# Kernel optimization log

Hardware: AMD Instinct MI355X
Metric: run time of the kernel (lower is better)

Reference implementation:

```python
import jax, jax.numpy as jnp
import numpy as np

N = 16384      # nodes
E = 262144     # edges (avg degree 16)
T = 4          # type_num
D = 64         # d_model
L = 2          # layers


def setup_inputs() -> dict:
    key = jax.random.key(0)
    ks = jax.random.split(key, 7)
    return {
        "x": jax.random.normal(ks[0], (N, D), dtype=jnp.float32),
        "edge_feature": jax.random.normal(ks[1], (T, D), dtype=jnp.float32),
        "theta": jax.random.normal(ks[2], (L, T, 3 * D), dtype=jnp.float32) * (1.0 / np.sqrt(3 * D)),
        "wr": jax.random.normal(ks[3], (L, D, D), dtype=jnp.float32) * (1.0 / np.sqrt(D)),
        "we": jax.random.normal(ks[4], (L, D, D), dtype=jnp.float32) * (1.0 / np.sqrt(D)),
        "edge_index": jax.random.randint(ks[5], (2, E), 0, N, dtype=jnp.int64),
        "edge_type": jax.random.randint(ks[6], (E,), 0, T, dtype=jnp.int64),
    }


def _scatter_softmax(r, row, num_nodes):
    # r: [T, E]; softmax over edges grouped by destination node `row`.
    rT = r.T  # [E, T] (segment ops reduce over leading axis)
    m = jax.ops.segment_max(rT, row, num_segments=num_nodes)   # [N, T]
    e = jnp.exp(rT - m[row])                                    # [E, T]
    s = jax.ops.segment_sum(e, row, num_segments=num_nodes)     # [N, T]
    return (e / s[row]).T                                       # [T, E]


def reference(x, edge_feature, theta, wr, we, edge_index, edge_type):
    n, d = x.shape
    t = edge_feature.shape[0]
    num_layers = theta.shape[0]
    row, col = edge_index[0], edge_index[1]

    h = jnp.broadcast_to(x[None], (t, n, d))  # x.expand(type_num, N, d)
    ef = edge_feature                          # [T, D]
    for i in range(num_layers):
        tg, thi, thj = theta[i, :, :d], theta[i, :, d:2 * d], theta[i, :, 2 * d:]
        # per-edge scores
        r_g = (tg @ ef.T)[:, edge_type]                        # [T, E]
        r_hi = jnp.einsum('tnd,td->tn', h, thi)[:, row]        # [T, E]
        r_hj = jnp.einsum('tnd,td->tn', h, thj)[:, col]        # [T, E]
        r = _scatter_softmax(r_g + r_hi + r_hj, row, n)        # [T, E]
        # gated messages
        ef = ef @ wr[i]                                        # [T, D]
        v_g = jax.nn.sigmoid(ef)[edge_type]                    # [E, D]
        v_h = jnp.einsum('tnd,de->tne', h, we[i])[:, col]      # [T, E, D]
        msg = r[:, :, None] * v_g[None] * v_h                  # [T, E, D]
        agg = jax.ops.segment_sum(jnp.moveaxis(msg, 1, 0), row, num_segments=n)  # [N, T, D]
        h = jnp.moveaxis(agg, 0, 1)                            # [T, N, D]
        if i < num_layers - 1:
            h = jax.nn.relu(h)      # dropout is identity in eval mode
            ef = jax.nn.relu(ef)
    return h
```

## Files before the change

kernel.cpp:

```cpp
#include <hip/hip_runtime.h>

#define NN 16384
#define EE 262144
#define TT 4
#define DD 64
#define SLOT 96
#define HB (EE / 256)
#define NB (NN / 64)

__device__ inline float wave_reduce_max(float v) {
    #pragma unroll
    for (int off = 32; off >= 1; off >>= 1) v = fmaxf(v, __shfl_xor(v, off));
    return v;
}
__device__ inline float wave_reduce_sum(float v) {
    #pragma unroll
    for (int off = 32; off >= 1; off >>= 1) v += __shfl_xor(v, off);
    return v;
}
__device__ inline float4 edge_group_reduce(float4 v) {
    #pragma unroll
    for (int off = 16; off < 64; off <<= 1) {
        v.x += __shfl_xor(v.x, off); v.y += __shfl_xor(v.y, off);
        v.z += __shfl_xor(v.z, off); v.w += __shfl_xor(v.w, off);
    }
    return v;
}
__device__ inline unsigned short f2bf(float f) {
    unsigned u = __float_as_uint(f);
    u += 0x7FFFu + ((u >> 16) & 1u);
    return (unsigned short)(u >> 16);
}
__device__ inline float bf2f(unsigned short h) {
    return __uint_as_float(((unsigned)h) << 16);
}
__device__ inline float4 bf4_to_f4(ushort4 h) {
    return float4{bf2f(h.x), bf2f(h.y), bf2f(h.z), bf2f(h.w)};
}

#define ONL(mm, ss, r) { if ((r) > (mm)) { ss = ss * __expf(mm - (r)) + 1.f; mm = (r); } \
                         else ss += __expf((r) - (mm)); }

__global__ __launch_bounds__(256) void build_node0_kernel(
        const int* __restrict__ row, const int* __restrict__ col,
        const int* __restrict__ et, int* __restrict__ cnt,
        int* __restrict__ ce_slot,
        const float* __restrict__ x, const float* __restrict__ theta,
        const float* __restrict__ we, const float* __restrict__ ef_in,
        const float* __restrict__ wr,
        float* __restrict__ a4, float* __restrict__ b4,
        unsigned short* __restrict__ hw0,
        float* __restrict__ sg, float* __restrict__ rg) {
    __shared__ float h_lds[64][68];
    __shared__ float4 we_lds[64][16];
    __shared__ float th_lds[4][2][64];
    __shared__ float part_a[64][4][4];
    __shared__ float part_b[64][4][4];
    __shared__ float ef0[TT * DD];
    __shared__ float ef1[TT * DD];
    int tid = threadIdx.x;
    int bid = blockIdx.x;

    if (bid < HB) {
        int e = bid * 256 + tid;
        int r = row[e];
        int pos = atomicAdd(&cnt[r], 1);
        if (pos < SLOT)
            ce_slot[r * SLOT + pos] = col[e] | (et[e] << 14);
        return;
    }
    bid -= HB;

    if (bid == NB) {
        int t = tid >> 6, d = tid & 63;
        ef0[tid] = ef_in[tid];
        __syncthreads();
        if (tid < 16) {
            int tt = tid & 3, tq = tid >> 2;
            float s = 0.f;
            for (int k = 0; k < DD; ++k) s += theta[tq * 192 + k] * ef0[tt * DD + k];
            rg[tq * 4 + tt] = s;
        }
        float acc = 0.f;
        for (int k = 0; k < DD; ++k) acc += ef0[t * DD + k] * wr[k * DD + d];
        sg[tid] = 1.f / (1.f + __expf(-acc));
        ef1[tid] = fmaxf(acc, 0.f);
        __syncthreads();
        if (tid < 16) {
            int tt = tid & 3, tq = tid >> 2;
            float s = 0.f;
            for (int k = 0; k < DD; ++k) s += theta[(TT + tq) * 192 + k] * ef1[tt * DD + k];
            rg[16 + tq * 4 + tt] = s;
        }
        float acc2 = 0.f;
        for (int k = 0; k < DD; ++k) acc2 += ef1[t * DD + k] * wr[DD * DD + k * DD + d];
        sg[TT * DD + tid] = 1.f / (1.f + __expf(-acc2));
        return;
    }

    int n0 = bid * 64;
    {
        int q = tid & 15, nr = tid >> 4;
        #pragma unroll
        for (int r = 0; r < 4; ++r) {
            int n = r * 16 + nr;
            *(float4*)&h_lds[n][4 * q] = ((const float4*)x)[(n0 + n) * 16 + q];
        }
    }
    {
        const float4* we4 = (const float4*)we;
        #pragma unroll
        for (int r = 0; r < 4; ++r)
            ((float4*)we_lds)[tid + 256 * r] = we4[tid + 256 * r];
    }
    {
        #pragma unroll
        for (int r = 0; r < 2; ++r) {
            int e = tid + 256 * r;
            int t = e >> 7, ab = (e >> 6) & 1, k = e & 63;
            th_lds[t][ab][k] = theta[t * 192 + 64 + ab * 64 + k];
        }
    }
    __syncthreads();
    int i = tid >> 4, j = tid & 15;
    float4 acc[4];
    acc[0] = acc[1] = acc[2] = acc[3] = float4{0.f, 0.f, 0.f, 0.f};
    for (int k = 0; k < 64; ++k) {
        float4 wv = we_lds[k][j];
        #pragma unroll
        for (int r = 0; r < 4; ++r) {
            float hv = h_lds[4 * i + r][k];
            acc[r].x += hv * wv.x; acc[r].y += hv * wv.y;
            acc[r].z += hv * wv.z; acc[r].w += hv * wv.w;
        }
    }
    {
        int t = j >> 2, kq = j & 3;
        float pa[4] = {0, 0, 0, 0}, pb[4] = {0, 0, 0, 0};
        for (int kk = 0; kk < 16; ++kk) {
            int k = kq * 16 + kk;
            float ti = th_lds[t][0][k], tj = th_lds[t][1][k];
            #pragma unroll
            for (int r = 0; r < 4; ++r) {
                float hv = h_lds[4 * i + r][k];
                pa[r] += hv * ti; pb[r] += hv * tj;
            }
        }
        #pragma unroll
        for (int r = 0; r < 4; ++r) {
            part_a[4 * i + r][t][kq] = pa[r];
            part_b[4 * i + r][t][kq] = pb[r];
        }
    }
    #pragma unroll
    for (int r = 0; r < 4; ++r) {
        ushort4 hv;
        hv.x = f2bf(acc[r].x); hv.y = f2bf(acc[r].y);
        hv.z = f2bf(acc[r].z); hv.w = f2bf(acc[r].w);
        ((ushort4*)hw0)[(n0 + 4 * i + r) * 16 + j] = hv;
    }
    __syncthreads();
    {
        int n = tid >> 2, t = tid & 3;
        float4 va = *(float4*)&part_a[n][t][0];
        float4 vb = *(float4*)&part_b[n][t][0];
        a4[(n0 + n) * 4 + t] = va.x + va.y + va.z + va.w;
        b4[(n0 + n) * 4 + t] = vb.x + vb.y + vb.z + vb.w;
    }
}

__global__ __launch_bounds__(256) void edge_agg0_kernel(
        const int* __restrict__ cnt, const int* __restrict__ ce_slot,
        const float* __restrict__ a4, const float* __restrict__ b4,
        const float* __restrict__ rg, const float* __restrict__ sg,
        const unsigned short* __restrict__ hw0,
        const float* __restrict__ we, const float* __restrict__ theta,
        float* __restrict__ a4o, float* __restrict__ b4o,
        unsigned short* __restrict__ hw1) {
    __shared__ float4 sg4[64];
    __shared__ float4 rg4[4];
    __shared__ int cols[4][SLOT];
    __shared__ float4 wT[4][SLOT];
    __shared__ float h1_lds[16][68];
    __shared__ float th1[4][2][64];
    __shared__ float part_a[16][17];
    __shared__ float part_b[16][17];
    int tid = threadIdx.x;
    if (tid < 64) sg4[tid] = ((const float4*)sg)[tid];
    if (tid < 4)  rg4[tid] = float4{rg[tid], rg[4 + tid], rg[8 + tid], rg[12 + tid]};
    #pragma unroll
    for (int r2 = 0; r2 < 2; ++r2) {
        int e2 = tid + 256 * r2;
        int t2 = e2 >> 7, ab = (e2 >> 6) & 1, k = e2 & 63;
        th1[t2][ab][k] = theta[(TT + t2) * 192 + 64 + ab * 64 + k];
    }
    int w = tid >> 6, lane = tid & 63;
    int n = blockIdx.x * 4 + w;
    int deg = cnt[n]; if (deg > SLOT) deg = SLOT;
    const int* ces = ce_slot + n * SLOT;
    float4 av = ((const float4*)a4)[n];
    __syncthreads();

    float m0 = -INFINITY, m1 = -INFINITY, m2 = -INFINITY, m3 = -INFINITY;
    float s0 = 0.f, s1 = 0.f, s2 = 0.f, s3 = 0.f;
    for (int e = lane; e < deg; e += 64) {
        int pk = ces[e];
        int c = pk & 16383, tt = pk >> 14;
        float4 bv = ((const float4*)b4)[c];
        float4 rv = rg4[tt];
        float4 rp{av.x + bv.x + rv.x, av.y + bv.y + rv.y,
                  av.z + bv.z + rv.z, av.w + bv.w + rv.w};
        cols[w][e] = pk;
        wT[w][e] = rp;
        ONL(m0, s0, rp.x) ONL(m1, s1, rp.y) ONL(m2, s2, rp.z) ONL(m3, s3, rp.w)
    }
    float M0 = wave_reduce_max(m0), M1 = wave_reduce_max(m1);
    float M2 = wave_reduce_max(m2), M3 = wave_reduce_max(m3);
    float S0 = wave_reduce_sum((m0 > -INFINITY) ? s0 * __expf(m0 - M0) : 0.f);
    float S1 = wave_reduce_sum((m1 > -INFINITY) ? s1 * __expf(m1 - M1) : 0.f);
    float S2 = wave_reduce_sum((m2 > -INFINITY) ? s2 * __expf(m2 - M2) : 0.f);
    float S3 = wave_reduce_sum((m3 > -INFINITY) ? s3 * __expf(m3 - M3) : 0.f);
    float i0 = (S0 > 0.f) ? 1.f / S0 : 0.f, i1 = (S1 > 0.f) ? 1.f / S1 : 0.f;
    float i2 = (S2 > 0.f) ? 1.f / S2 : 0.f, i3 = (S3 > 0.f) ? 1.f / S3 : 0.f;
    for (int e = lane; e < deg; e += 64) {
        float4 rp = wT[w][e];
        wT[w][e] = float4{__expf(rp.x - M0) * i0, __expf(rp.y - M1) * i1,
                          __expf(rp.z - M2) * i2, __expf(rp.w - M3) * i3};
    }

    int eg = lane >> 4, q = lane & 15;
    float4 acc0{0,0,0,0}, acc1{0,0,0,0}, acc2{0,0,0,0}, acc3{0,0,0,0};
    const ushort4* hw4 = (const ushort4*)hw0;
    for (int base = 0; base < deg; base += 4) {
        int e = base + eg;
        if (e < deg) {
            int pk = cols[w][e];
            int c = pk & 16383, tt = pk >> 14;
            ushort4 hv = hw4[c * 16 + q];
            float4 sgv = sg4[tt * 16 + q];
            float4 wv = wT[w][e];
            float4 f = bf4_to_f4(hv);
            float4 g{sgv.x * f.x, sgv.y * f.y, sgv.z * f.z, sgv.w * f.w};
            acc0.x += wv.x * g.x; acc0.y += wv.x * g.y; acc0.z += wv.x * g.z; acc0.w += wv.x * g.w;
            acc1.x += wv.y * g.x; acc1.y += wv.y * g.y; acc1.z += wv.y * g.z; acc1.w += wv.y * g.w;
            acc2.x += wv.z * g.x; acc2.y += wv.z * g.y; acc2.z += wv.z * g.z; acc2.w += wv.z * g.w;
            acc3.x += wv.w * g.x; acc3.y += wv.w * g.y; acc3.z += wv.w * g.z; acc3.w += wv.w * g.w;
        }
    }
    acc0 = edge_group_reduce(acc0);
    acc1 = edge_group_reduce(acc1);
    acc2 = edge_group_reduce(acc2);
    acc3 = edge_group_reduce(acc3);
    float4 o = acc0;
    if (eg == 1) o = acc1;
    if (eg == 2) o = acc2;
    if (eg == 3) o = acc3;
    o.x = fmaxf(o.x, 0.f); o.y = fmaxf(o.y, 0.f);
    o.z = fmaxf(o.z, 0.f); o.w = fmaxf(o.w, 0.f);
    *(float4*)&h1_lds[eg * 4 + w][4 * q] = o;
    __syncthreads();

    int r = tid >> 4, j = tid & 15;
    int t1 = r >> 2, wn = r & 3;
    int n1 = blockIdx.x * 4 + wn;
    const float4* we2 = (const float4*)(we + DD * DD);
    float4 ga{0,0,0,0};
    for (int k = 0; k < 64; ++k) {
        float hv = h1_lds[r][k];
        float4 wv = we2[k * 16 + j];
        ga.x += hv * wv.x; ga.y += hv * wv.y;
        ga.z += hv * wv.z; ga.w += hv * wv.w;
    }
    float pa = 0.f, pb = 0.f;
    #pragma unroll
    for (int kk = 0; kk < 4; ++kk) {
        int k = 4 * j + kk;
        float hv = h1_lds[r][k];
        pa += hv * th1[t1][0][k]; pb += hv * th1[t1][1][k];
    }
    part_a[r][j] = pa; part_b[r][j] = pb;
    ushort4 hb;
    hb.x = f2bf(ga.x); hb.y = f2bf(ga.y); hb.z = f2bf(ga.z); hb.w = f2bf(ga.w);
    ((ushort4*)hw1)[((size_t)t1 * NN + n1) * 16 + j] = hb;
    __syncthreads();
    if (tid < 16) {
        float s = 0.f;
        #pragma unroll
        for (int jj = 0; jj < 16; ++jj) s += part_a[tid][jj];
        a4o[(blockIdx.x * 4 + (tid & 3)) * 4 + (tid >> 2)] = s;
    } else if (tid < 32) {
        int r3 = tid - 16;
        float s = 0.f;
        #pragma unroll
        for (int jj = 0; jj < 16; ++jj) s += part_b[r3][jj];
        b4o[(blockIdx.x * 4 + (r3 & 3)) * 4 + (r3 >> 2)] = s;
    }
}

__global__ __launch_bounds__(256) void edge_agg1_kernel(
        const int* __restrict__ cnt, const int* __restrict__ ce_slot,
        const float* __restrict__ a4, const float* __restrict__ b4,
        const float* __restrict__ rg, const float* __restrict__ sg,
        const unsigned short* __restrict__ hw, float* __restrict__ out) {
    __shared__ float4 sg4[64];
    __shared__ float4 rg4[4];
    __shared__ int cols[4][SLOT];
    __shared__ float4 wT[4][SLOT];
    int tid = threadIdx.x;
    if (tid < 64) sg4[tid] = ((const float4*)sg)[tid];
    if (tid < 4)  rg4[tid] = float4{rg[tid], rg[4 + tid], rg[8 + tid], rg[12 + tid]};
    int w = tid >> 6, lane = tid & 63;
    int n = blockIdx.x * 4 + w;
    int deg = cnt[n]; if (deg > SLOT) deg = SLOT;
    const int* ces = ce_slot + n * SLOT;
    float4 av = ((const float4*)a4)[n];
    __syncthreads();

    float m0 = -INFINITY, m1 = -INFINITY, m2 = -INFINITY, m3 = -INFINITY;
    float s0 = 0.f, s1 = 0.f, s2 = 0.f, s3 = 0.f;
    for (int e = lane; e < deg; e += 64) {
        int pk = ces[e];
        int c = pk & 16383, tt = pk >> 14;
        float4 bv = ((const float4*)b4)[c];
        float4 rv = rg4[tt];
        float4 rp{av.x + bv.x + rv.x, av.y + bv.y + rv.y,
                  av.z + bv.z + rv.z, av.w + bv.w + rv.w};
        cols[w][e] = pk;
        wT[w][e] = rp;
        ONL(m0, s0, rp.x) ONL(m1, s1, rp.y) ONL(m2, s2, rp.z) ONL(m3, s3, rp.w)
    }
    float M0 = wave_reduce_max(m0), M1 = wave_reduce_max(m1);
    float M2 = wave_reduce_max(m2), M3 = wave_reduce_max(m3);
    float S0 = wave_reduce_sum((m0 > -INFINITY) ? s0 * __expf(m0 - M0) : 0.f);
    float S1 = wave_reduce_sum((m1 > -INFINITY) ? s1 * __expf(m1 - M1) : 0.f);
    float S2 = wave_reduce_sum((m2 > -INFINITY) ? s2 * __expf(m2 - M2) : 0.f);
    float S3 = wave_reduce_sum((m3 > -INFINITY) ? s3 * __expf(m3 - M3) : 0.f);
    float i0 = (S0 > 0.f) ? 1.f / S0 : 0.f, i1 = (S1 > 0.f) ? 1.f / S1 : 0.f;
    float i2 = (S2 > 0.f) ? 1.f / S2 : 0.f, i3 = (S3 > 0.f) ? 1.f / S3 : 0.f;
    for (int e = lane; e < deg; e += 64) {
        float4 rp = wT[w][e];
        wT[w][e] = float4{__expf(rp.x - M0) * i0, __expf(rp.y - M1) * i1,
                          __expf(rp.z - M2) * i2, __expf(rp.w - M3) * i3};
    }

    int eg = lane >> 4, q = lane & 15;
    float4 acc0{0,0,0,0}, acc1{0,0,0,0}, acc2{0,0,0,0}, acc3{0,0,0,0};
    const ushort4* hw4 = (const ushort4*)hw;
    for (int base = 0; base < deg; base += 4) {
        int e = base + eg;
        if (e < deg) {
            int pk = cols[w][e];
            int c = pk & 16383, tt = pk >> 14;
            int ba = c * 16 + q;
            ushort4 h0 = hw4[ba];
            ushort4 h1v = hw4[NN * 16 + ba];
            ushort4 h2 = hw4[2 * NN * 16 + ba];
            ushort4 h3 = hw4[3 * NN * 16 + ba];
            float4 sgv = sg4[tt * 16 + q];
            float4 wv = wT[w][e];
            float4 f0 = bf4_to_f4(h0), f1 = bf4_to_f4(h1v);
            float4 f2 = bf4_to_f4(h2), f3 = bf4_to_f4(h3);
            acc0.x += wv.x * sgv.x * f0.x; acc0.y += wv.x * sgv.y * f0.y;
            acc0.z += wv.x * sgv.z * f0.z; acc0.w += wv.x * sgv.w * f0.w;
            acc1.x += wv.y * sgv.x * f1.x; acc1.y += wv.y * sgv.y * f1.y;
            acc1.z += wv.y * sgv.z * f1.z; acc1.w += wv.y * sgv.w * f1.w;
            acc2.x += wv.z * sgv.x * f2.x; acc2.y += wv.z * sgv.y * f2.y;
            acc2.z += wv.z * sgv.z * f2.z; acc2.w += wv.z * sgv.w * f2.w;
            acc3.x += wv.w * sgv.x * f3.x; acc3.y += wv.w * sgv.y * f3.y;
            acc3.z += wv.w * sgv.z * f3.z; acc3.w += wv.w * sgv.w * f3.w;
        }
    }
    acc0 = edge_group_reduce(acc0);
    acc1 = edge_group_reduce(acc1);
    acc2 = edge_group_reduce(acc2);
    acc3 = edge_group_reduce(acc3);
    float4 o = acc0;
    if (eg == 1) o = acc1;
    if (eg == 2) o = acc2;
    if (eg == 3) o = acc3;
    ((float4*)out)[(eg * NN + n) * 16 + q] = o;
}

extern "C" void kernel_launch(void* const* d_in, const int* in_sizes, int n_in,
                              void* d_out, int out_size, void* d_ws, size_t ws_size,
                              hipStream_t stream) {
    const float* x     = (const float*)d_in[0];
    const float* ef_in = (const float*)d_in[1];
    const float* theta = (const float*)d_in[2];
    const float* wr    = (const float*)d_in[3];
    const float* we    = (const float*)d_in[4];
    const int* edge_index = (const int*)d_in[5];
    const int* edge_type  = (const int*)d_in[6];
    float* out = (float*)d_out;

    const int* row = edge_index;
    const int* col = edge_index + EE;

    char* p = (char*)d_ws;
    auto alloc = [&](size_t bytes) { void* r = (void*)p; p += (bytes + 255) & ~(size_t)255; return r; };
    int*   cnt     = (int*)  alloc((size_t)NN * 4);
    int*   ce_slot = (int*)  alloc((size_t)NN * SLOT * 4);
    float* a4_0    = (float*)alloc((size_t)NN * 4 * 4);
    float* b4_0    = (float*)alloc((size_t)NN * 4 * 4);
    float* a4_1    = (float*)alloc((size_t)NN * 4 * 4);
    float* b4_1    = (float*)alloc((size_t)NN * 4 * 4);
    unsigned short* hw0 = (unsigned short*)alloc((size_t)NN * DD * 2);
    unsigned short* hw1 = (unsigned short*)alloc((size_t)TT * NN * DD * 2);
    float* sg      = (float*)alloc((size_t)2 * TT * DD * 4);
    float* rg      = (float*)alloc((size_t)2 * 16 * 4);

    hipMemsetAsync(cnt, 0, (size_t)NN * 4, stream);
    build_node0_kernel<<<HB + NB + 1, 256, 0, stream>>>(
        row, col, edge_type, cnt, ce_slot, x, theta, we, ef_in, wr,
        a4_0, b4_0, hw0, sg, rg);
    edge_agg0_kernel<<<NN / 4, 256, 0, stream>>>(
        cnt, ce_slot, a4_0, b4_0, rg, sg, hw0, we, theta, a4_1, b4_1, hw1);
    edge_agg1_kernel<<<NN / 4, 256, 0, stream>>>(
        cnt, ce_slot, a4_1, b4_1, rg + 16, sg + TT * DD, hw1, out);
}
```

Measured before the change: 156.8 us.

## Split layer-1 node transform out of edge aggregation into a tiled kernel

The layer-0 edge aggregation kernel no longer computes the layer-1 node transform (h1·We and the theta projections) inline. It now writes relu'd h1 in fp32 to global memory, and a new node1_kernel tiles 64 nodes per block with We and theta staged in LDS to compute hw1, a4 and b4. This removes the per-block global reads of We with poor reuse and the extra syncs and LDS pressure in the aggregation kernel. In exchange it adds a 16 MB fp32 round trip through global memory and one more kernel launch.

```diff
diff --git a/kernel.cpp b/kernel.cpp
--- a/kernel.cpp
+++ b/kernel.cpp
@@ -169,31 +169,103 @@
     }
 }
 
+__global__ __launch_bounds__(256) void node1_kernel(
+        const float* __restrict__ h1, const float* __restrict__ theta,
+        const float* __restrict__ we,
+        float* __restrict__ a4, float* __restrict__ b4,
+        unsigned short* __restrict__ hw) {
+    __shared__ float h_lds[64][68];
+    __shared__ float4 we_lds[64][16];
+    __shared__ float th_lds[2][64];
+    __shared__ float part_a[64][17];
+    __shared__ float part_b[64][17];
+    int tid = threadIdx.x;
+    int t = blockIdx.y;
+    int n0 = blockIdx.x * 64;
+    const float* ht = h1 + (size_t)t * NN * DD;
+    {
+        int q = tid & 15, nr = tid >> 4;
+        #pragma unroll
+        for (int r = 0; r < 4; ++r) {
+            int n = r * 16 + nr;
+            *(float4*)&h_lds[n][4 * q] = ((const float4*)ht)[(n0 + n) * 16 + q];
+        }
+    }
+    {
+        const float4* we4 = (const float4*)(we + DD * DD);
+        #pragma unroll
+        for (int r = 0; r < 4; ++r)
+            ((float4*)we_lds)[tid + 256 * r] = we4[tid + 256 * r];
+    }
+    if (tid < 128) {
+        int ab = tid >> 6, k = tid & 63;
+        th_lds[ab][k] = theta[(TT + t) * 192 + 64 + ab * 64 + k];
+    }
+    __syncthreads();
+    int i = tid >> 4, j = tid & 15;
+    float4 acc[4];
+    acc[0] = acc[1] = acc[2] = acc[3] = float4{0.f, 0.f, 0.f, 0.f};
+    for (int k = 0; k < 64; ++k) {
+        float4 wv = we_lds[k][j];
+        #pragma unroll
+        for (int r = 0; r < 4; ++r) {
+            float hv = h_lds[4 * i + r][k];
+            acc[r].x += hv * wv.x; acc[r].y += hv * wv.y;
+            acc[r].z += hv * wv.z; acc[r].w += hv * wv.w;
+        }
+    }
+    {
+        float pa[4] = {0, 0, 0, 0}, pb[4] = {0, 0, 0, 0};
+        #pragma unroll
+        for (int kk = 0; kk < 4; ++kk) {
+            int k = 4 * j + kk;
+            float ti = th_lds[0][k], tj = th_lds[1][k];
+            #pragma unroll
+            for (int r = 0; r < 4; ++r) {
+                float hv = h_lds[4 * i + r][k];
+                pa[r] += hv * ti; pb[r] += hv * tj;
+            }
+        }
+        #pragma unroll
+        for (int r = 0; r < 4; ++r) {
+            part_a[4 * i + r][j] = pa[r];
+            part_b[4 * i + r][j] = pb[r];
+        }
+    }
+    #pragma unroll
+    for (int r = 0; r < 4; ++r) {
+        ushort4 hv;
+        hv.x = f2bf(acc[r].x); hv.y = f2bf(acc[r].y);
+        hv.z = f2bf(acc[r].z); hv.w = f2bf(acc[r].w);
+        ((ushort4*)hw)[((size_t)t * NN + n0 + 4 * i + r) * 16 + j] = hv;
+    }
+    __syncthreads();
+    if (tid < 64) {
+        float s = 0.f;
+        #pragma unroll
+        for (int jj = 0; jj < 16; ++jj) s += part_a[tid][jj];
+        a4[(n0 + tid) * 4 + t] = s;
+    } else if (tid < 128) {
+        int n = tid - 64;
+        float s = 0.f;
+        #pragma unroll
+        for (int jj = 0; jj < 16; ++jj) s += part_b[n][jj];
+        b4[(n0 + n) * 4 + t] = s;
+    }
+}
+
 __global__ __launch_bounds__(256) void edge_agg0_kernel(
         const int* __restrict__ cnt, const int* __restrict__ ce_slot,
         const float* __restrict__ a4, const float* __restrict__ b4,
         const float* __restrict__ rg, const float* __restrict__ sg,
-        const unsigned short* __restrict__ hw0,
-        const float* __restrict__ we, const float* __restrict__ theta,
-        float* __restrict__ a4o, float* __restrict__ b4o,
-        unsigned short* __restrict__ hw1) {
+        const unsigned short* __restrict__ hw0, float* __restrict__ h1) {
     __shared__ float4 sg4[64];
     __shared__ float4 rg4[4];
     __shared__ int cols[4][SLOT];
     __shared__ float4 wT[4][SLOT];
-    __shared__ float h1_lds[16][68];
-    __shared__ float th1[4][2][64];
-    __shared__ float part_a[16][17];
-    __shared__ float part_b[16][17];
     int tid = threadIdx.x;
     if (tid < 64) sg4[tid] = ((const float4*)sg)[tid];
     if (tid < 4)  rg4[tid] = float4{rg[tid], rg[4 + tid], rg[8 + tid], rg[12 + tid]};
-    #pragma unroll
-    for (int r2 = 0; r2 < 2; ++r2) {
-        int e2 = tid + 256 * r2;
-        int t2 = e2 >> 7, ab = (e2 >> 6) & 1, k = e2 & 63;
-        th1[t2][ab][k] = theta[(TT + t2) * 192 + 64 + ab * 64 + k];
-    }
     int w = tid >> 6, lane = tid & 63;
     int n = blockIdx.x * 4 + w;
     int deg = cnt[n]; if (deg > SLOT) deg = SLOT;
@@ -257,44 +329,7 @@
     if (eg == 3) o = acc3;
     o.x = fmaxf(o.x, 0.f); o.y = fmaxf(o.y, 0.f);
     o.z = fmaxf(o.z, 0.f); o.w = fmaxf(o.w, 0.f);
-    *(float4*)&h1_lds[eg * 4 + w][4 * q] = o;
-    __syncthreads();
-
-    int r = tid >> 4, j = tid & 15;
-    int t1 = r >> 2, wn = r & 3;
-    int n1 = blockIdx.x * 4 + wn;
-    const float4* we2 = (const float4*)(we + DD * DD);
-    float4 ga{0,0,0,0};
-    for (int k = 0; k < 64; ++k) {
-        float hv = h1_lds[r][k];
-        float4 wv = we2[k * 16 + j];
-        ga.x += hv * wv.x; ga.y += hv * wv.y;
-        ga.z += hv * wv.z; ga.w += hv * wv.w;
-    }
-    float pa = 0.f, pb = 0.f;
-    #pragma unroll
-    for (int kk = 0; kk < 4; ++kk) {
-        int k = 4 * j + kk;
-        float hv = h1_lds[r][k];
-        pa += hv * th1[t1][0][k]; pb += hv * th1[t1][1][k];
-    }
-    part_a[r][j] = pa; part_b[r][j] = pb;
-    ushort4 hb;
-    hb.x = f2bf(ga.x); hb.y = f2bf(ga.y); hb.z = f2bf(ga.z); hb.w = f2bf(ga.w);
-    ((ushort4*)hw1)[((size_t)t1 * NN + n1) * 16 + j] = hb;
-    __syncthreads();
-    if (tid < 16) {
-        float s = 0.f;
-        #pragma unroll
-        for (int jj = 0; jj < 16; ++jj) s += part_a[tid][jj];
-        a4o[(blockIdx.x * 4 + (tid & 3)) * 4 + (tid >> 2)] = s;
-    } else if (tid < 32) {
-        int r3 = tid - 16;
-        float s = 0.f;
-        #pragma unroll
-        for (int jj = 0; jj < 16; ++jj) s += part_b[r3][jj];
-        b4o[(blockIdx.x * 4 + (r3 & 3)) * 4 + (r3 >> 2)] = s;
-    }
+    ((float4*)h1)[(eg * NN + n) * 16 + q] = o;
 }
 
 __global__ __launch_bounds__(256) void edge_agg1_kernel(
@@ -406,6 +441,7 @@
     float* b4_1    = (float*)alloc((size_t)NN * 4 * 4);
     unsigned short* hw0 = (unsigned short*)alloc((size_t)NN * DD * 2);
     unsigned short* hw1 = (unsigned short*)alloc((size_t)TT * NN * DD * 2);
+    float* h1      = (float*)alloc((size_t)TT * NN * DD * 4);
     float* sg      = (float*)alloc((size_t)2 * TT * DD * 4);
     float* rg      = (float*)alloc((size_t)2 * 16 * 4);
 
@@ -414,7 +450,9 @@
         row, col, edge_type, cnt, ce_slot, x, theta, we, ef_in, wr,
         a4_0, b4_0, hw0, sg, rg);
     edge_agg0_kernel<<<NN / 4, 256, 0, stream>>>(
-        cnt, ce_slot, a4_0, b4_0, rg, sg, hw0, we, theta, a4_1, b4_1, hw1);
+        cnt, ce_slot, a4_0, b4_0, rg, sg, hw0, h1);
+    node1_kernel<<<dim3(NN / 64, TT), 256, 0, stream>>>(
+        h1, theta, we, a4_1, b4_1, hw1);
     edge_agg1_kernel<<<NN / 4, 256, 0, stream>>>(
         cnt, ce_slot, a4_1, b4_1, rg + 16, sg + TT * DD, hw1, out);
 }
```

Measured after the change: 147.4 us. 6.0% less time.
